# Optimization experiments

Measured on AMD Instinct MI355X. Metric: run time of the kernel, lower is better.

Reference implementation:

```python
import jax, jax.numpy as jnp
import numpy as np

V, M, N, C, H, OUT = 50000, 16, 8, 8, 4, 256
DK = OUT // H  # 64


def setup_inputs() -> dict:
    key = jax.random.key(0)
    ks = jax.random.split(key, 9)
    return {
        "x": jax.random.normal(ks[0], (V, C * N), dtype=jnp.float32),
        "neighbors": jax.random.randint(ks[1], (V, M), 0, V, dtype=jnp.int64),
        "parallel_transport_matrices": jax.random.normal(ks[2], (V, M, N, N), dtype=jnp.float32),
        "rel_pos_u": jax.random.normal(ks[3], (V, M, 2), dtype=jnp.float32),
        "W_Q_w": jax.random.normal(ks[4], (OUT, C * N), dtype=jnp.float32) * 0.05,
        "W_Q_b": jnp.zeros((OUT,), dtype=jnp.float32),
        "W_K_w": jax.random.normal(ks[5], (OUT, C * N), dtype=jnp.float32) * 0.05,
        "W_K_b": jnp.zeros((OUT,), dtype=jnp.float32),
        "kernel_bases": jax.random.normal(ks[6], (6, N, N), dtype=jnp.float32),
        "kernel_coeffs": jax.random.normal(ks[7], (H, 6), dtype=jnp.float32),
    }


def reference(x, neighbors, parallel_transport_matrices, rel_pos_u,
              W_Q_w, W_Q_b, W_K_w, W_K_b, kernel_bases, kernel_coeffs):
    Nv = x.shape[0]
    # gather neighbor features and split channel axis: [V, M, C, N]
    x_neigh = x[neighbors].reshape(Nv, M, C, N)
    # parallel transport: [V,M,N,N] x [V,M,C,N] -> [V,M,N,C]
    f_prime = jnp.einsum('vnoj,vnpj->vnop', parallel_transport_matrices, x_neigh)
    f_prime_flat = f_prime.reshape(Nv, M, C * N)  # row-major flatten (as torch)
    # queries / keys
    Q = (x @ W_Q_w.T + W_Q_b).reshape(Nv, H, DK)
    K = (f_prime_flat @ W_K_w.T + W_K_b).reshape(Nv, M, H, DK)
    scores = jnp.einsum('vhd,vnhd->vnh', Q, K) / np.float32(np.sqrt(DK))
    attn = jax.nn.softmax(scores, axis=1)  # softmax over neighbors
    # learned value transform from fixed kernel bases: [H,N,N]
    W_V = jnp.einsum('hb,bij->hij', kernel_coeffs, kernel_bases)
    f_split = f_prime_flat.reshape(Nv, M, C, N)
    # values: [V,M,H,C,N] -> [V,M,H,C*N]
    values = jnp.einsum('hij,vncj->vnhci', W_V, f_split).reshape(Nv, M, H, C * N)
    out = jnp.einsum('vnh,vnhd->vhd', attn, values)
    return out.reshape(Nv, H * C * N)
```

## Files before the change

kernel.cpp:

```cpp
#include <hip/hip_runtime.h>
#include <hip/hip_bf16.h>

#define NV 50000


typedef _Float16 h2_t __attribute__((ext_vector_type(2)));
typedef _Float16 f16x8 __attribute__((ext_vector_type(8)));
typedef float f32x4 __attribute__((ext_vector_type(4)));
typedef unsigned u32x4 __attribute__((ext_vector_type(4)));

#if defined(__has_builtin)
#if __has_builtin(__builtin_amdgcn_fdot2)
#define HAVE_FDOT2 1
#endif
#endif

__device__ __forceinline__ float fdot2f(h2_t a, h2_t b, float c) {
#ifdef HAVE_FDOT2
  return __builtin_amdgcn_fdot2(a, b, c, false);
#else
  return fmaf((float)a.x, (float)b.x, fmaf((float)a.y, (float)b.y, c));
#endif
}
__device__ __forceinline__ h2_t u2h(unsigned u) {
  union { unsigned u; h2_t h; } c; c.u = u; return c.h;
}
__device__ __forceinline__ unsigned pk2(float a, float b) {
  auto v = __builtin_amdgcn_cvt_pkrtz(a, b);
  union { decltype(v) h; unsigned u; } c; c.h = v; return c.u;
}
__device__ __forceinline__ f16x8 u4h8(uint4 u) {
  union { uint4 u; f16x8 h; } c; c.u = u; return c.h;
}
__device__ __forceinline__ void lds_fence() {
  asm volatile("s_waitcnt lgkmcnt(0)" ::: "memory");
  __builtin_amdgcn_sched_barrier(0);
}

__global__ void prep_kernel(const float* __restrict__ WQ, const float* __restrict__ WQb,
                            const float* __restrict__ WK,
                            const float* __restrict__ bases, const float* __restrict__ coeffs,
                            const float* __restrict__ x,
                            unsigned* __restrict__ AhTs, float* __restrict__ rbar,
                            unsigned* __restrict__ wvh, unsigned* __restrict__ xh) {
  if (blockIdx.x < 32) {
    int ep = blockIdx.x;
    int od = threadIdx.x;
    int h = od >> 6, d = od & 63;
    int e0 = ep * 2;
    float s0 = 0.f, s1 = 0.f;
#pragma unroll 4
    for (int k = 0; k < 64; ++k) {
      float wk = WK[(h * 64 + k) * 64 + d];
      s0 += WQ[(h * 64 + k) * 64 + e0] * wk;
      s1 += WQ[(h * 64 + k) * 64 + e0 + 1] * wk;
    }
    AhTs[((ep >> 2) * 256 + od) * 4 + (ep & 3)] = pk2(s0 * 0.125f, s1 * 0.125f);
    if (ep == 0) {
      float r = 0.f;
      for (int k = 0; k < 64; ++k) r += WQb[h * 64 + k] * WK[(h * 64 + k) * 64 + d];
      rbar[od] = r * 0.125f;
      if (od < 128) {
        int i = od >> 4, hh = (od >> 2) & 3, jp = od & 3;
        float w0 = 0.f, w1 = 0.f;
        for (int b = 0; b < 6; ++b) {
          w0 += coeffs[hh * 6 + b] * bases[b * 64 + i * 8 + 2 * jp];
          w1 += coeffs[hh * 6 + b] * bases[b * 64 + i * 8 + 2 * jp + 1];
        }
        wvh[od] = pk2(w0, w1);
      }
    }
  } else {
    int idx = (blockIdx.x - 32) * 256 + threadIdx.x;
    if (idx < NV * 8) {
      float4 a = ((const float4*)x)[idx * 2];
      float4 b = ((const float4*)x)[idx * 2 + 1];
      uint4 o;
      o.x = pk2(a.x, a.y);
      o.y = pk2(a.z, a.w);
      o.z = pk2(b.x, b.y);
      o.w = pk2(b.z, b.w);
      ((uint4*)xh)[idx] = o;
    }
  }
}

__device__ __forceinline__ void gload_lds16(const void* g, void* l) {
  __builtin_amdgcn_global_load_lds((const __attribute__((address_space(1))) void*)g,
                                   (__attribute__((address_space(3))) void*)l, 16, 0, 0);
}

__global__ __launch_bounds__(256, 6) void attn_kernel(
    const unsigned* __restrict__ xh, const int* __restrict__ nbr,
    const float* __restrict__ P, const unsigned* __restrict__ AhTs,
    const float* __restrict__ rbar, const unsigned* __restrict__ wvh,
    float* __restrict__ out) {
  __shared__ __align__(16) _Float16 UN[4][2048];
  __shared__ __align__(16) _Float16 q16[4][256];
  __shared__ __align__(16) float    attn_lds[4][64];
  __shared__ __align__(16) _Float16 g16[4][4][64];

  const int t = threadIdx.x;
  const int w = t >> 6, lane = t & 63;
  const int v0 = blockIdx.x * 4;
  const int v = v0 + w;
  const int o = lane >> 3, p = lane & 7;
  const int c_ep = lane >> 3, i_ep = lane & 7;
  const char* xhb = (const char*)xh;

  int nbi0 = nbr[(size_t)v * 16 + (lane >> 3)];
  int nbi1 = nbr[(size_t)v * 16 + 8 + (lane >> 3)];

  u32x4 c0, c1, c2, c3;
  {
    const u32x4* Pg = (const u32x4*)(P + (size_t)v * 1024);
    c0 = __builtin_nontemporal_load(Pg + lane);
    c1 = __builtin_nontemporal_load(Pg + 64 + lane);
    c2 = __builtin_nontemporal_load(Pg + 128 + lane);
    c3 = __builtin_nontemporal_load(Pg + 192 + lane);
  }

  gload_lds16(xhb + (size_t)nbi0 * 128 + (lane & 7) * 16, &UN[w][1024]);
  gload_lds16(xhb + (size_t)nbi1 * 128 + (lane & 7) * 16, &UN[w][1536]);

  float rbq[4];
#pragma unroll
  for (int tt = 0; tt < 4; ++tt) rbq[tt] = rbar[w * 64 + tt * 16 + (lane & 15)];

  {
    uint2 w0, w1, w2, w3;
    w0.x = pk2(__uint_as_float(c0[0]), __uint_as_float(c0[1]));
    w0.y = pk2(__uint_as_float(c0[2]), __uint_as_float(c0[3]));
    w1.x = pk2(__uint_as_float(c1[0]), __uint_as_float(c1[1]));
    w1.y = pk2(__uint_as_float(c1[2]), __uint_as_float(c1[3]));
    w2.x = pk2(__uint_as_float(c2[0]), __uint_as_float(c2[1]));
    w2.y = pk2(__uint_as_float(c2[2]), __uint_as_float(c2[3]));
    w3.x = pk2(__uint_as_float(c3[0]), __uint_as_float(c3[1]));
    w3.y = pk2(__uint_as_float(c3[2]), __uint_as_float(c3[3]));
    *(uint2*)&UN[w][lane * 4]       = w0;
    *(uint2*)&UN[w][256 + lane * 4] = w1;
    *(uint2*)&UN[w][512 + lane * 4] = w2;
    *(uint2*)&UN[w][768 + lane * 4] = w3;
  }

  {
    const int od0 = w * 64;
    const uint4* xrow4 = (const uint4*)(xh + (size_t)(v0 + (lane & 3)) * 32);
    f16x8 afrag0 = u4h8(xrow4[(lane >> 4)]);
    f16x8 afrag1 = u4h8(xrow4[4 + (lane >> 4)]);

    f32x4 acc[4];
#pragma unroll
    for (int tt = 0; tt < 4; ++tt) acc[tt] = (f32x4){0.f, 0.f, 0.f, 0.f};

#pragma unroll
    for (int tt = 0; tt < 4; ++tt) {
      const int colbase = od0 + tt * 16 + (lane & 15);
#pragma unroll
      for (int s = 0; s < 2; ++s) {
        uint4 bu = *(const uint4*)&AhTs[((s * 4 + (lane >> 4)) * 256 + colbase) * 4];
        acc[tt] = __builtin_amdgcn_mfma_f32_16x16x32_f16(s ? afrag1 : afrag0, u4h8(bu),
                                                         acc[tt], 0, 0, 0);
      }
    }
    if (lane < 16) {
#pragma unroll
      for (int tt = 0; tt < 4; ++tt)
#pragma unroll
        for (int vi = 0; vi < 4; ++vi)
          q16[vi][od0 + tt * 16 + lane] = (_Float16)(acc[tt][vi] + rbq[tt]);
    }
  }
  __syncthreads();

  const int hb = (lane & 15) & 3;
  f16x8 bq0 = u4h8(*(const uint4*)&q16[w][hb * 64 + (lane >> 4) * 8]);
  f16x8 bq1 = u4h8(*(const uint4*)&q16[w][hb * 64 + 32 + (lane >> 4) * 8]);

  const uint4* P16 = (const uint4*)&UN[w][0];
  const uint4* X16 = (const uint4*)&UN[w][1024];
  float freg[16];
#pragma unroll
  for (int m = 0; m < 16; ++m) {
    uint4 Pu = P16[m * 8 + o];
    uint4 Xu = X16[m * 8 + p];
    freg[m] = fdot2f(u2h(Pu.x), u2h(Xu.x),
              fdot2f(u2h(Pu.y), u2h(Xu.y),
              fdot2f(u2h(Pu.z), u2h(Xu.z),
              fdot2f(u2h(Pu.w), u2h(Xu.w), 0.f))));
  }
  lds_fence();

#pragma unroll
  for (int m = 0; m < 16; ++m) UN[w][m * 72 + lane] = (_Float16)freg[m];
  lds_fence();

  f32x4 sac = (f32x4){0.f, 0.f, 0.f, 0.f};
  {
    f16x8 af0 = u4h8(*(const uint4*)&UN[w][(lane & 15) * 72 + (lane >> 4) * 8]);
    f16x8 af1 = u4h8(*(const uint4*)&UN[w][(lane & 15) * 72 + 32 + (lane >> 4) * 8]);
    sac = __builtin_amdgcn_mfma_f32_16x16x32_f16(af0, bq0, sac, 0, 0, 0);
    sac = __builtin_amdgcn_mfma_f32_16x16x32_f16(af1, bq1, sac, 0, 0, 0);
  }

  {
    float e0 = __expf(sac[0]), e1 = __expf(sac[1]);
    float e2 = __expf(sac[2]), e3 = __expf(sac[3]);
    if ((lane & 15) < 4) {
      const int h = lane & 15, mb = (lane >> 4) * 4;
      attn_lds[w][(mb + 0) * 4 + h] = e0;
      attn_lds[w][(mb + 1) * 4 + h] = e1;
      attn_lds[w][(mb + 2) * 4 + h] = e2;
      attn_lds[w][(mb + 3) * 4 + h] = e3;
    }
  }
  lds_fence();

  uint4 wq[4];
#pragma unroll
  for (int h = 0; h < 4; ++h) wq[h] = *(const uint4*)&wvh[i_ep * 16 + h * 4];

  float g[4] = {0.f, 0.f, 0.f, 0.f};
  float s4[4] = {0.f, 0.f, 0.f, 0.f};
#pragma unroll
  for (int m = 0; m < 16; ++m) {
    float4 a4 = *(const float4*)&attn_lds[w][m * 4];
    g[0] = fmaf(a4.x, freg[m], g[0]);
    g[1] = fmaf(a4.y, freg[m], g[1]);
    g[2] = fmaf(a4.z, freg[m], g[2]);
    g[3] = fmaf(a4.w, freg[m], g[3]);
    s4[0] += a4.x; s4[1] += a4.y; s4[2] += a4.z; s4[3] += a4.w;
  }

#pragma unroll
  for (int h = 0; h < 4; ++h) g16[w][h][lane] = (_Float16)(g[h] / s4[h]);
  lds_fence();
#pragma unroll
  for (int h = 0; h < 4; ++h) {
    uint4 gq = *(const uint4*)&g16[w][h][c_ep * 8];
    float oacc = fdot2f(u2h(wq[h].x), u2h(gq.x),
                 fdot2f(u2h(wq[h].y), u2h(gq.y),
                 fdot2f(u2h(wq[h].z), u2h(gq.z),
                 fdot2f(u2h(wq[h].w), u2h(gq.w), 0.f))));
    __builtin_nontemporal_store(oacc, &out[(size_t)v * 256 + h * 64 + lane]);
  }
}

extern "C" void kernel_launch(void* const* d_in, const int* in_sizes, int n_in,
                              void* d_out, int out_size, void* d_ws, size_t ws_size,
                              hipStream_t stream) {
  const float* x      = (const float*)d_in[0];
  const int*   nbr    = (const int*)d_in[1];
  const float* P      = (const float*)d_in[2];
  const float* WQ     = (const float*)d_in[4];
  const float* WQb    = (const float*)d_in[5];
  const float* WK     = (const float*)d_in[6];
  const float* bases  = (const float*)d_in[8];
  const float* coeffs = (const float*)d_in[9];

  unsigned* AhTs = (unsigned*)d_ws;
  float* rbar   = (float*)((char*)d_ws + 32768);
  unsigned* wvh = (unsigned*)((char*)d_ws + 33792);
  unsigned* xh  = (unsigned*)((char*)d_ws + 34816);
  float* out    = (float*)d_out;

  hipLaunchKernelGGL(prep_kernel, dim3(32 + (NV * 8 + 255) / 256), dim3(256), 0, stream,
                     WQ, WQb, WK, bases, coeffs, x, AhTs, rbar, wvh, xh);
  hipLaunchKernelGGL(attn_kernel, dim3(NV / 4), dim3(256), 0, stream,
                     xh, nbr, P, AhTs, rbar, wvh, out);
}
```

Measured before the change: 81.60 us.

## Process two vertices per wave with prefetched transport matrices and shared weight loads

Each block now handles 8 vertices, so each wave processes two vertices in sequence. All global loads (neighbor indices, transport matrices, gathered features) for both vertices are issued up front, so the second vertex's memory traffic overlaps the first vertex's compute. The W_Q fragments are loaded once and reused for two query MFMA batches, and transported features move to a separate LDS buffer so the second P tile can be staged early. In exchange it uses more registers and LDS (launch bounds drop from 6 to 4 blocks per CU), which lowers occupancy.

```diff
diff --git a/kernel.cpp b/kernel.cpp
--- a/kernel.cpp
+++ b/kernel.cpp
@@ -90,38 +90,48 @@
                                    (__attribute__((address_space(3))) void*)l, 16, 0, 0);
 }
 
-__global__ __launch_bounds__(256, 6) void attn_kernel(
+__global__ __launch_bounds__(256, 4) void attn_kernel(
     const unsigned* __restrict__ xh, const int* __restrict__ nbr,
     const float* __restrict__ P, const unsigned* __restrict__ AhTs,
     const float* __restrict__ rbar, const unsigned* __restrict__ wvh,
     float* __restrict__ out) {
-  __shared__ __align__(16) _Float16 UN[4][2048];
-  __shared__ __align__(16) _Float16 q16[4][256];
+  __shared__ __align__(16) _Float16 UN[4][3072];
+  __shared__ __align__(16) _Float16 Ftr[4][1152];
+  __shared__ __align__(16) _Float16 q16[8][256];
   __shared__ __align__(16) float    attn_lds[4][64];
   __shared__ __align__(16) _Float16 g16[4][4][64];
 
   const int t = threadIdx.x;
   const int w = t >> 6, lane = t & 63;
-  const int v0 = blockIdx.x * 4;
-  const int v = v0 + w;
+  const int v0 = blockIdx.x * 8;
+  const int va = v0 + w, vb = v0 + 4 + w;
   const int o = lane >> 3, p = lane & 7;
   const int c_ep = lane >> 3, i_ep = lane & 7;
   const char* xhb = (const char*)xh;
 
-  int nbi0 = nbr[(size_t)v * 16 + (lane >> 3)];
-  int nbi1 = nbr[(size_t)v * 16 + 8 + (lane >> 3)];
-
-  u32x4 c0, c1, c2, c3;
-  {
-    const u32x4* Pg = (const u32x4*)(P + (size_t)v * 1024);
-    c0 = __builtin_nontemporal_load(Pg + lane);
-    c1 = __builtin_nontemporal_load(Pg + 64 + lane);
-    c2 = __builtin_nontemporal_load(Pg + 128 + lane);
-    c3 = __builtin_nontemporal_load(Pg + 192 + lane);
-  }
-
-  gload_lds16(xhb + (size_t)nbi0 * 128 + (lane & 7) * 16, &UN[w][1024]);
-  gload_lds16(xhb + (size_t)nbi1 * 128 + (lane & 7) * 16, &UN[w][1536]);
+  int nbA0 = nbr[(size_t)va * 16 + (lane >> 3)];
+  int nbA1 = nbr[(size_t)va * 16 + 8 + (lane >> 3)];
+  int nbB0 = nbr[(size_t)vb * 16 + (lane >> 3)];
+  int nbB1 = nbr[(size_t)vb * 16 + 8 + (lane >> 3)];
+
+  u32x4 a0, a1, a2, a3, b0, b1, b2, b3;
+  {
+    const u32x4* PgA = (const u32x4*)(P + (size_t)va * 1024);
+    const u32x4* PgB = (const u32x4*)(P + (size_t)vb * 1024);
+    a0 = __builtin_nontemporal_load(PgA + lane);
+    a1 = __builtin_nontemporal_load(PgA + 64 + lane);
+    a2 = __builtin_nontemporal_load(PgA + 128 + lane);
+    a3 = __builtin_nontemporal_load(PgA + 192 + lane);
+    b0 = __builtin_nontemporal_load(PgB + lane);
+    b1 = __builtin_nontemporal_load(PgB + 64 + lane);
+    b2 = __builtin_nontemporal_load(PgB + 128 + lane);
+    b3 = __builtin_nontemporal_load(PgB + 192 + lane);
+  }
+
+  gload_lds16(xhb + (size_t)nbA0 * 128 + (lane & 7) * 16, &UN[w][1024]);
+  gload_lds16(xhb + (size_t)nbA1 * 128 + (lane & 7) * 16, &UN[w][1536]);
+  gload_lds16(xhb + (size_t)nbB0 * 128 + (lane & 7) * 16, &UN[w][2048]);
+  gload_lds16(xhb + (size_t)nbB1 * 128 + (lane & 7) * 16, &UN[w][2560]);
 
   float rbq[4];
 #pragma unroll
@@ -129,14 +139,14 @@
 
   {
     uint2 w0, w1, w2, w3;
-    w0.x = pk2(__uint_as_float(c0[0]), __uint_as_float(c0[1]));
-    w0.y = pk2(__uint_as_float(c0[2]), __uint_as_float(c0[3]));
-    w1.x = pk2(__uint_as_float(c1[0]), __uint_as_float(c1[1]));
-    w1.y = pk2(__uint_as_float(c1[2]), __uint_as_float(c1[3]));
-    w2.x = pk2(__uint_as_float(c2[0]), __uint_as_float(c2[1]));
-    w2.y = pk2(__uint_as_float(c2[2]), __uint_as_float(c2[3]));
-    w3.x = pk2(__uint_as_float(c3[0]), __uint_as_float(c3[1]));
-    w3.y = pk2(__uint_as_float(c3[2]), __uint_as_float(c3[3]));
+    w0.x = pk2(__uint_as_float(a0[0]), __uint_as_float(a0[1]));
+    w0.y = pk2(__uint_as_float(a0[2]), __uint_as_float(a0[3]));
+    w1.x = pk2(__uint_as_float(a1[0]), __uint_as_float(a1[1]));
+    w1.y = pk2(__uint_as_float(a1[2]), __uint_as_float(a1[3]));
+    w2.x = pk2(__uint_as_float(a2[0]), __uint_as_float(a2[1]));
+    w2.y = pk2(__uint_as_float(a2[2]), __uint_as_float(a2[3]));
+    w3.x = pk2(__uint_as_float(a3[0]), __uint_as_float(a3[1]));
+    w3.y = pk2(__uint_as_float(a3[2]), __uint_as_float(a3[3]));
     *(uint2*)&UN[w][lane * 4]       = w0;
     *(uint2*)&UN[w][256 + lane * 4] = w1;
     *(uint2*)&UN[w][512 + lane * 4] = w2;
@@ -145,64 +155,110 @@
 
   {
     const int od0 = w * 64;
-    const uint4* xrow4 = (const uint4*)(xh + (size_t)(v0 + (lane & 3)) * 32);
-    f16x8 afrag0 = u4h8(xrow4[(lane >> 4)]);
-    f16x8 afrag1 = u4h8(xrow4[4 + (lane >> 4)]);
-
-    f32x4 acc[4];
-#pragma unroll
-    for (int tt = 0; tt < 4; ++tt) acc[tt] = (f32x4){0.f, 0.f, 0.f, 0.f};
-
-#pragma unroll
-    for (int tt = 0; tt < 4; ++tt) {
-      const int colbase = od0 + tt * 16 + (lane & 15);
-#pragma unroll
-      for (int s = 0; s < 2; ++s) {
-        uint4 bu = *(const uint4*)&AhTs[((s * 4 + (lane >> 4)) * 256 + colbase) * 4];
-        acc[tt] = __builtin_amdgcn_mfma_f32_16x16x32_f16(s ? afrag1 : afrag0, u4h8(bu),
-                                                         acc[tt], 0, 0, 0);
+    uint4 bu[2][4];
+#pragma unroll
+    for (int s = 0; s < 2; ++s)
+#pragma unroll
+      for (int tt = 0; tt < 4; ++tt)
+        bu[s][tt] = *(const uint4*)&AhTs[((s * 4 + (lane >> 4)) * 256 + od0 + tt * 16 + (lane & 15)) * 4];
+
+    {
+      const uint4* xr = (const uint4*)(xh + (size_t)(v0 + (lane & 3)) * 32);
+      f16x8 af0 = u4h8(xr[(lane >> 4)]);
+      f16x8 af1 = u4h8(xr[4 + (lane >> 4)]);
+      f32x4 acc[4];
+#pragma unroll
+      for (int tt = 0; tt < 4; ++tt) acc[tt] = (f32x4){0.f, 0.f, 0.f, 0.f};
+#pragma unroll
+      for (int tt = 0; tt < 4; ++tt)
+#pragma unroll
+        for (int s = 0; s < 2; ++s)
+          acc[tt] = __builtin_amdgcn_mfma_f32_16x16x32_f16(s ? af1 : af0, u4h8(bu[s][tt]),
+                                                           acc[tt], 0, 0, 0);
+      if (lane < 16) {
+#pragma unroll
+        for (int tt = 0; tt < 4; ++tt)
+#pragma unroll
+          for (int vi = 0; vi < 4; ++vi)
+            q16[vi][od0 + tt * 16 + lane] = (_Float16)(acc[tt][vi] + rbq[tt]);
       }
     }
-    if (lane < 16) {
+    {
+      const uint4* xr = (const uint4*)(xh + (size_t)(v0 + 4 + (lane & 3)) * 32);
+      f16x8 af0 = u4h8(xr[(lane >> 4)]);
+      f16x8 af1 = u4h8(xr[4 + (lane >> 4)]);
+      f32x4 acc[4];
+#pragma unroll
+      for (int tt = 0; tt < 4; ++tt) acc[tt] = (f32x4){0.f, 0.f, 0.f, 0.f};
 #pragma unroll
       for (int tt = 0; tt < 4; ++tt)
 #pragma unroll
-        for (int vi = 0; vi < 4; ++vi)
-          q16[vi][od0 + tt * 16 + lane] = (_Float16)(acc[tt][vi] + rbq[tt]);
+        for (int s = 0; s < 2; ++s)
+          acc[tt] = __builtin_amdgcn_mfma_f32_16x16x32_f16(s ? af1 : af0, u4h8(bu[s][tt]),
+                                                           acc[tt], 0, 0, 0);
+      if (lane < 16) {
+#pragma unroll
+        for (int tt = 0; tt < 4; ++tt)
+#pragma unroll
+          for (int vi = 0; vi < 4; ++vi)
+            q16[4 + vi][od0 + tt * 16 + lane] = (_Float16)(acc[tt][vi] + rbq[tt]);
+      }
     }
   }
   __syncthreads();
 
+  uint4 wq[4];
+#pragma unroll
+  for (int h = 0; h < 4; ++h) wq[h] = *(const uint4*)&wvh[i_ep * 16 + h * 4];
+
   const int hb = (lane & 15) & 3;
+  const int rowA = (lane & 15) * 72 + (lane >> 4) * 8;
+
   f16x8 bq0 = u4h8(*(const uint4*)&q16[w][hb * 64 + (lane >> 4) * 8]);
   f16x8 bq1 = u4h8(*(const uint4*)&q16[w][hb * 64 + 32 + (lane >> 4) * 8]);
 
-  const uint4* P16 = (const uint4*)&UN[w][0];
-  const uint4* X16 = (const uint4*)&UN[w][1024];
   float freg[16];
-#pragma unroll
-  for (int m = 0; m < 16; ++m) {
-    uint4 Pu = P16[m * 8 + o];
-    uint4 Xu = X16[m * 8 + p];
-    freg[m] = fdot2f(u2h(Pu.x), u2h(Xu.x),
-              fdot2f(u2h(Pu.y), u2h(Xu.y),
-              fdot2f(u2h(Pu.z), u2h(Xu.z),
-              fdot2f(u2h(Pu.w), u2h(Xu.w), 0.f))));
-  }
-  lds_fence();
-
-#pragma unroll
-  for (int m = 0; m < 16; ++m) UN[w][m * 72 + lane] = (_Float16)freg[m];
+  {
+    const uint4* P16 = (const uint4*)&UN[w][0];
+    const uint4* X16 = (const uint4*)&UN[w][1024];
+#pragma unroll
+    for (int m = 0; m < 16; ++m) {
+      uint4 Pu = P16[m * 8 + o];
+      uint4 Xu = X16[m * 8 + p];
+      freg[m] = fdot2f(u2h(Pu.x), u2h(Xu.x),
+                fdot2f(u2h(Pu.y), u2h(Xu.y),
+                fdot2f(u2h(Pu.z), u2h(Xu.z),
+                fdot2f(u2h(Pu.w), u2h(Xu.w), 0.f))));
+    }
+  }
+  lds_fence();
+
+#pragma unroll
+  for (int m = 0; m < 16; ++m) Ftr[w][m * 72 + lane] = (_Float16)freg[m];
+  {
+    uint2 w0, w1, w2, w3;
+    w0.x = pk2(__uint_as_float(b0[0]), __uint_as_float(b0[1]));
+    w0.y = pk2(__uint_as_float(b0[2]), __uint_as_float(b0[3]));
+    w1.x = pk2(__uint_as_float(b1[0]), __uint_as_float(b1[1]));
+    w1.y = pk2(__uint_as_float(b1[2]), __uint_as_float(b1[3]));
+    w2.x = pk2(__uint_as_float(b2[0]), __uint_as_float(b2[1]));
+    w2.y = pk2(__uint_as_float(b2[2]), __uint_as_float(b2[3]));
+    w3.x = pk2(__uint_as_float(b3[0]), __uint_as_float(b3[1]));
+    w3.y = pk2(__uint_as_float(b3[2]), __uint_as_float(b3[3]));
+    *(uint2*)&UN[w][lane * 4]       = w0;
+    *(uint2*)&UN[w][256 + lane * 4] = w1;
+    *(uint2*)&UN[w][512 + lane * 4] = w2;
+    *(uint2*)&UN[w][768 + lane * 4] = w3;
+  }
   lds_fence();
 
   f32x4 sac = (f32x4){0.f, 0.f, 0.f, 0.f};
   {
-    f16x8 af0 = u4h8(*(const uint4*)&UN[w][(lane & 15) * 72 + (lane >> 4) * 8]);
-    f16x8 af1 = u4h8(*(const uint4*)&UN[w][(lane & 15) * 72 + 32 + (lane >> 4) * 8]);
+    f16x8 af0 = u4h8(*(const uint4*)&Ftr[w][rowA]);
+    f16x8 af1 = u4h8(*(const uint4*)&Ftr[w][rowA + 32]);
     sac = __builtin_amdgcn_mfma_f32_16x16x32_f16(af0, bq0, sac, 0, 0, 0);
     sac = __builtin_amdgcn_mfma_f32_16x16x32_f16(af1, bq1, sac, 0, 0, 0);
   }
-
   {
     float e0 = __expf(sac[0]), e1 = __expf(sac[1]);
     float e2 = __expf(sac[2]), e3 = __expf(sac[3]);
@@ -216,24 +272,21 @@
   }
   lds_fence();
 
-  uint4 wq[4];
-#pragma unroll
-  for (int h = 0; h < 4; ++h) wq[h] = *(const uint4*)&wvh[i_ep * 16 + h * 4];
-
-  float g[4] = {0.f, 0.f, 0.f, 0.f};
-  float s4[4] = {0.f, 0.f, 0.f, 0.f};
-#pragma unroll
-  for (int m = 0; m < 16; ++m) {
-    float4 a4 = *(const float4*)&attn_lds[w][m * 4];
-    g[0] = fmaf(a4.x, freg[m], g[0]);
-    g[1] = fmaf(a4.y, freg[m], g[1]);
-    g[2] = fmaf(a4.z, freg[m], g[2]);
-    g[3] = fmaf(a4.w, freg[m], g[3]);
-    s4[0] += a4.x; s4[1] += a4.y; s4[2] += a4.z; s4[3] += a4.w;
-  }
-
-#pragma unroll
-  for (int h = 0; h < 4; ++h) g16[w][h][lane] = (_Float16)(g[h] / s4[h]);
+  {
+    float g[4] = {0.f, 0.f, 0.f, 0.f};
+    float s4[4] = {0.f, 0.f, 0.f, 0.f};
+#pragma unroll
+    for (int m = 0; m < 16; ++m) {
+      float4 a4 = *(const float4*)&attn_lds[w][m * 4];
+      g[0] = fmaf(a4.x, freg[m], g[0]);
+      g[1] = fmaf(a4.y, freg[m], g[1]);
+      g[2] = fmaf(a4.z, freg[m], g[2]);
+      g[3] = fmaf(a4.w, freg[m], g[3]);
+      s4[0] += a4.x; s4[1] += a4.y; s4[2] += a4.z; s4[3] += a4.w;
+    }
+#pragma unroll
+    for (int h = 0; h < 4; ++h) g16[w][h][lane] = (_Float16)(g[h] / s4[h]);
+  }
   lds_fence();
 #pragma unroll
   for (int h = 0; h < 4; ++h) {
@@ -242,7 +295,73 @@
                  fdot2f(u2h(wq[h].y), u2h(gq.y),
                  fdot2f(u2h(wq[h].z), u2h(gq.z),
                  fdot2f(u2h(wq[h].w), u2h(gq.w), 0.f))));
-    __builtin_nontemporal_store(oacc, &out[(size_t)v * 256 + h * 64 + lane]);
+    __builtin_nontemporal_store(oacc, &out[(size_t)va * 256 + h * 64 + lane]);
+  }
+
+  bq0 = u4h8(*(const uint4*)&q16[4 + w][hb * 64 + (lane >> 4) * 8]);
+  bq1 = u4h8(*(const uint4*)&q16[4 + w][hb * 64 + 32 + (lane >> 4) * 8]);
+
+  {
+    const uint4* P16 = (const uint4*)&UN[w][0];
+    const uint4* X16 = (const uint4*)&UN[w][2048];
+#pragma unroll
+    for (int m = 0; m < 16; ++m) {
+      uint4 Pu = P16[m * 8 + o];
+      uint4 Xu = X16[m * 8 + p];
+      freg[m] = fdot2f(u2h(Pu.x), u2h(Xu.x),
+                fdot2f(u2h(Pu.y), u2h(Xu.y),
+                fdot2f(u2h(Pu.z), u2h(Xu.z),
+                fdot2f(u2h(Pu.w), u2h(Xu.w), 0.f))));
+    }
+  }
+#pragma unroll
+  for (int m = 0; m < 16; ++m) Ftr[w][m * 72 + lane] = (_Float16)freg[m];
+  lds_fence();
+
+  sac = (f32x4){0.f, 0.f, 0.f, 0.f};
+  {
+    f16x8 af0 = u4h8(*(const uint4*)&Ftr[w][rowA]);
+    f16x8 af1 = u4h8(*(const uint4*)&Ftr[w][rowA + 32]);
+    sac = __builtin_amdgcn_mfma_f32_16x16x32_f16(af0, bq0, sac, 0, 0, 0);
+    sac = __builtin_amdgcn_mfma_f32_16x16x32_f16(af1, bq1, sac, 0, 0, 0);
+  }
+  {
+    float e0 = __expf(sac[0]), e1 = __expf(sac[1]);
+    float e2 = __expf(sac[2]), e3 = __expf(sac[3]);
+    if ((lane & 15) < 4) {
+      const int h = lane & 15, mb = (lane >> 4) * 4;
+      attn_lds[w][(mb + 0) * 4 + h] = e0;
+      attn_lds[w][(mb + 1) * 4 + h] = e1;
+      attn_lds[w][(mb + 2) * 4 + h] = e2;
+      attn_lds[w][(mb + 3) * 4 + h] = e3;
+    }
+  }
+  lds_fence();
+
+  {
+    float g[4] = {0.f, 0.f, 0.f, 0.f};
+    float s4[4] = {0.f, 0.f, 0.f, 0.f};
+#pragma unroll
+    for (int m = 0; m < 16; ++m) {
+      float4 a4 = *(const float4*)&attn_lds[w][m * 4];
+      g[0] = fmaf(a4.x, freg[m], g[0]);
+      g[1] = fmaf(a4.y, freg[m], g[1]);
+      g[2] = fmaf(a4.z, freg[m], g[2]);
+      g[3] = fmaf(a4.w, freg[m], g[3]);
+      s4[0] += a4.x; s4[1] += a4.y; s4[2] += a4.z; s4[3] += a4.w;
+    }
+#pragma unroll
+    for (int h = 0; h < 4; ++h) g16[w][h][lane] = (_Float16)(g[h] / s4[h]);
+  }
+  lds_fence();
+#pragma unroll
+  for (int h = 0; h < 4; ++h) {
+    uint4 gq = *(const uint4*)&g16[w][h][c_ep * 8];
+    float oacc = fdot2f(u2h(wq[h].x), u2h(gq.x),
+                 fdot2f(u2h(wq[h].y), u2h(gq.y),
+                 fdot2f(u2h(wq[h].z), u2h(gq.z),
+                 fdot2f(u2h(wq[h].w), u2h(gq.w), 0.f))));
+    __builtin_nontemporal_store(oacc, &out[(size_t)vb * 256 + h * 64 + lane]);
   }
 }
 
@@ -266,6 +385,6 @@
 
   hipLaunchKernelGGL(prep_kernel, dim3(32 + (NV * 8 + 255) / 256), dim3(256), 0, stream,
                      WQ, WQb, WK, bases, coeffs, x, AhTs, rbar, wvh, xh);
-  hipLaunchKernelGGL(attn_kernel, dim3(NV / 4), dim3(256), 0, stream,
+  hipLaunchKernelGGL(attn_kernel, dim3(NV / 8), dim3(256), 0, stream,
                      xh, nbr, P, AhTs, rbar, wvh, out);
 }
```

Measured after the change: 78.15 us. -4.2%, faster.
